# Kernel tuning notes

Hardware: AMD Instinct MI355X
Metric: run time of the kernel (lower is better)

Reference implementation:

```python
import jax, jax.numpy as jnp
import numpy as np

DIM = 1024
NUM_EXPERTS = 8
ACTIVE_EXPERTS = 2
EXPERT_DIM = 2048


def setup_inputs() -> dict:
    key = jax.random.key(0)
    k1, k2, k3, k4 = jax.random.split(key, 4)
    x = jax.random.normal(k1, (1, 2048, DIM), dtype=jnp.float32)
    gate_w = jax.random.normal(k2, (NUM_EXPERTS, DIM), dtype=jnp.float32) * 0.02
    balance_bias = jnp.zeros((NUM_EXPERTS,), dtype=jnp.float32)
    w1 = jax.random.normal(k3, (NUM_EXPERTS, EXPERT_DIM, DIM), dtype=jnp.float32) * 0.02
    w2 = jax.random.normal(k4, (NUM_EXPERTS, DIM, EXPERT_DIM), dtype=jnp.float32) * 0.02
    return {"x": x, "gate_w": gate_w, "balance_bias": balance_bias, "w1": w1, "w2": w2}


def reference(x, gate_w, balance_bias, w1, w2):
    B, S, D = x.shape
    T = B * S
    xf = x.reshape(T, D)
    # gating: sigmoid scores with load-balance bias, then top-k
    gate_logits = jnp.einsum('td,ed->te', xf, gate_w)
    gate_scores = jax.nn.sigmoid(gate_logits + balance_bias)
    topk_scores, topk_idx = jax.lax.top_k(gate_scores, ACTIVE_EXPERTS)
    topk_scores = topk_scores / (topk_scores.sum(axis=-1, keepdims=True) + 1e-6)
    # scatter normalized scores into dense combine weights [T, E]
    comb = jnp.zeros((T, NUM_EXPERTS), dtype=x.dtype)
    comb = comb.at[jnp.arange(T)[:, None], topk_idx].add(topk_scores)
    # expert FFNs (dense over experts; combine weight zeroes unselected)
    h = jax.nn.silu(jnp.einsum('td,ehd->teh', xf, w1))   # [T, E, expert_dim]
    expert_out = jnp.einsum('teh,edh->ted', h, w2)        # [T, E, D]
    out = jnp.einsum('te,ted->td', comb, expert_out)
    return out.reshape(B, S, D)
```

## Files before the change

### kernel.cpp

```cpp
#include <hip/hip_runtime.h>

#define T 2048
#define DIM 1024
#define NE 8
#define ED 2048
#define PSLOT 5120
#define MT_MAX 16

#define BM 128
#define BN 64
#define BK 32

typedef __attribute__((ext_vector_type(8))) short s8v;
typedef __attribute__((ext_vector_type(4))) float f32x4;

__device__ __forceinline__ short f2bf(float f) {
    union { float f; unsigned u; } v;
    v.f = f;
    unsigned r = 0x7FFFu + ((v.u >> 16) & 1u);
    v.u += r;
    return (short)(v.u >> 16);
}

__device__ __forceinline__ float bf2f(short s) {
    union { unsigned u; float f; } v;
    v.u = ((unsigned)(unsigned short)s) << 16;
    return v.f;
}

__device__ __forceinline__ unsigned pkbf2(float lo, float hi) {
    union { float f; unsigned u; } a, b;
    a.f = lo; b.f = hi;
    return __builtin_amdgcn_perm(b.u + 0x8000u, a.u + 0x8000u, 0x07060302u);
}

__device__ __forceinline__ void glds16(const void* g, void* l) {
    __builtin_amdgcn_global_load_lds(
        (const __attribute__((address_space(1))) void*)g,
        (__attribute__((address_space(3))) void*)l, 16, 0, 0);
}

__global__ __launch_bounds__(256) void convert1_kernel(const float* __restrict__ w1,
                                                       short* __restrict__ wbt) {
    int wid = blockIdx.x * 4 + (threadIdx.x >> 6);
    int lane = threadIdx.x & 63;
    int e = wid >> 10, rem = wid & 1023, nb = rem >> 5, kk = rem & 31;
    const float4* src = (const float4*)(w1 + ((size_t)(e * ED + nb * 64 + lane)) * DIM + kk * 32);
    short* dst = wbt + ((size_t)(e * 32 + nb) * 128 + kk * 4) * 512 + lane * 8;
#pragma unroll
    for (int q = 0; q < 4; ++q) {
        float4 f0 = src[2 * q], f1 = src[2 * q + 1];
        uint4 o = { pkbf2(f0.x, f0.y), pkbf2(f0.z, f0.w), pkbf2(f1.x, f1.y), pkbf2(f1.z, f1.w) };
        *(uint4*)(dst + q * 512) = o;
    }
}

__global__ __launch_bounds__(256) void convert2_kernel(const float* __restrict__ w2,
                                                       short* __restrict__ wbt) {
    int wid = blockIdx.x * 4 + (threadIdx.x >> 6);
    int lane = threadIdx.x & 63;
    int e = wid >> 10, rem = wid & 1023, nb = rem >> 6, kk = rem & 63;
    const float4* src = (const float4*)(w2 + ((size_t)(e * DIM + nb * 64 + lane)) * ED + kk * 32);
    short* dst = wbt + ((size_t)(e * 16 + nb) * 256 + kk * 4) * 512 + lane * 8;
#pragma unroll
    for (int q = 0; q < 4; ++q) {
        float4 f0 = src[2 * q], f1 = src[2 * q + 1];
        uint4 o = { pkbf2(f0.x, f0.y), pkbf2(f0.z, f0.w), pkbf2(f1.x, f1.y), pkbf2(f1.z, f1.w) };
        *(uint4*)(dst + q * 512) = o;
    }
}

__global__ void router_kernel(const float* __restrict__ x,
                              const float* __restrict__ gw,
                              const float* __restrict__ bias,
                              int* __restrict__ counts,
                              int* __restrict__ top2i,
                              float* __restrict__ top2w) {
    int wid = threadIdx.x >> 6;
    int lane = threadIdx.x & 63;
    int t = blockIdx.x * 4 + wid;

    const float* xr = x + (size_t)t * DIM + lane * 16;
    float4 xv[4];
#pragma unroll
    for (int j = 0; j < 4; ++j) xv[j] = *(const float4*)(xr + j * 4);

    float sc[NE];
#pragma unroll
    for (int e = 0; e < NE; ++e) {
        const float* gr = gw + e * DIM + lane * 16;
        float p = 0.f;
#pragma unroll
        for (int j = 0; j < 4; ++j) {
            float4 g = *(const float4*)(gr + j * 4);
            p += xv[j].x * g.x + xv[j].y * g.y + xv[j].z * g.z + xv[j].w * g.w;
        }
#pragma unroll
        for (int off = 32; off; off >>= 1) p += __shfl_xor(p, off, 64);
        sc[e] = 1.f / (1.f + __expf(-(p + bias[e])));
    }
    int b0 = 0; float s0 = sc[0];
#pragma unroll
    for (int e = 1; e < NE; ++e) if (sc[e] > s0) { s0 = sc[e]; b0 = e; }
    int b1 = -1; float s1 = -1e30f;
#pragma unroll
    for (int e = 0; e < NE; ++e) if (e != b0 && sc[e] > s1) { s1 = sc[e]; b1 = e; }
    float inv = 1.f / (s0 + s1 + 1e-6f);
    if (lane == 0) {
        top2i[t * 2 + 0] = b0; top2i[t * 2 + 1] = b1;
        top2w[t * 2 + 0] = s0 * inv; top2w[t * 2 + 1] = s1 * inv;
        atomicAdd(&counts[b0], 1);
        atomicAdd(&counts[b1], 1);
    }
}

__global__ __launch_bounds__(256) void plan_kernel(
    const int* __restrict__ counts, const int* __restrict__ top2i,
    int* __restrict__ poff, int* __restrict__ tok_list, int* __restrict__ slot_of) {
    __shared__ int soff[NE];
    __shared__ int srun[NE];
    if (threadIdx.x == 0) {
        int a = 0;
        for (int e = 0; e < NE; ++e) {
            soff[e] = a; poff[e] = a;
            a += ((counts[e] + 127) >> 7) << 7;
            srun[e] = 0;
        }
    }
    __syncthreads();
    for (int t = threadIdx.x; t < T; t += 256) {
#pragma unroll
        for (int k = 0; k < 2; ++k) {
            int e = top2i[t * 2 + k];
            int pos = atomicAdd(&srun[e], 1);
            int slot = soff[e] + pos;
            tok_list[slot] = t;
            slot_of[t * 2 + k] = slot;
        }
    }
    __syncthreads();
    for (int e = 0; e < NE; ++e) {
        int cnt = counts[e];
        int lim = ((cnt + 127) >> 7) << 7;
        for (int i = cnt + threadIdx.x; i < lim; i += 256) tok_list[soff[e] + i] = 0;
    }
}

__global__ __launch_bounds__(256) void gather_kernel(
    const float* __restrict__ x, const int* __restrict__ counts,
    const int* __restrict__ poff, const int* __restrict__ tok_list,
    short* __restrict__ xgt) {
    int e = blockIdx.x, mb = blockIdx.y;
    int cnt = counts[e];
    int mt = (cnt + 127) >> 7;
    if (mb >= mt) return;
    int pb = (poff[e] >> 7) + mb;
    int r = threadIdx.x & 127, hh = threadIdx.x >> 7;
    int tok = tok_list[poff[e] + mb * 128 + r];
    const float4* src = (const float4*)(x + (size_t)tok * DIM + hh * 16);
    short* dst = xgt + ((size_t)pb * 128 + hh * 2) * 1024 + r * 8;
#pragma unroll 4
    for (int kk = 0; kk < DIM / 32; ++kk) {
        float4 f0 = src[0], f1 = src[1], f2 = src[2], f3 = src[3];
        uint4 o0 = { pkbf2(f0.x, f0.y), pkbf2(f0.z, f0.w), pkbf2(f1.x, f1.y), pkbf2(f1.z, f1.w) };
        uint4 o1 = { pkbf2(f2.x, f2.y), pkbf2(f2.z, f2.w), pkbf2(f3.x, f3.y), pkbf2(f3.z, f3.w) };
        *(uint4*)(dst) = o0;
        *(uint4*)(dst + 1024) = o1;
        src += 8;
        dst += 4 * 1024;
    }
}

__global__ __launch_bounds__(256) void ffn1_kernel(
    const short* __restrict__ xgt, const short* __restrict__ wbt,
    const int* __restrict__ counts, const int* __restrict__ poff,
    short* __restrict__ ht) {
    int e = blockIdx.x & 7;
    int j = blockIdx.x >> 3;
    int cnt = counts[e];
    int mt = (cnt + 127) >> 7;
    const int NT = ED / BN;
    if (j >= mt * NT) return;
    int mb = j / NT, nb = j % NT;
    int pb = (poff[e] >> 7) + mb;

    __shared__ __align__(16) short As[2][4][BM][8];
    __shared__ __align__(16) short Bs[2][4][BN][8];

    int tid = threadIdx.x;
    int lane = tid & 63, w = tid >> 6;
    int mo = w * 32;
    int lrow = lane & 15, lq = lane >> 4;

    f32x4 acc[2][4];
#pragma unroll
    for (int mi = 0; mi < 2; ++mi)
#pragma unroll
        for (int ni = 0; ni < 4; ++ni) acc[mi][ni] = (f32x4){0.f, 0.f, 0.f, 0.f};

    const short* asrc = xgt + (size_t)pb * 128 * 1024;
    const short* bsrc = wbt + (size_t)(e * 32 + nb) * 128 * 512;

    auto stage = [&](int s, int b) {
        int p = s * 4 + w;
        glds16(asrc + (size_t)p * 1024 + lane * 8,       &As[b][w][0][0]);
        glds16(asrc + (size_t)p * 1024 + 512 + lane * 8, &As[b][w][64][0]);
        glds16(bsrc + (size_t)p * 512 + lane * 8,        &Bs[b][w][0][0]);
    };
    const int NK = DIM / BK;
    stage(0, 0);
    for (int kk = 0; kk < NK; ++kk) {
        int cur = kk & 1, nxt = cur ^ 1;
        __syncthreads();
        if (kk + 1 < NK) stage(kk + 1, nxt);
        s8v af[2], bfr[4];
#pragma unroll
        for (int mi = 0; mi < 2; ++mi) af[mi] = *(const s8v*)&As[cur][lq][mo + mi * 16 + lrow][0];
#pragma unroll
        for (int ni = 0; ni < 4; ++ni) bfr[ni] = *(const s8v*)&Bs[cur][lq][ni * 16 + lrow][0];
#pragma unroll
        for (int mi = 0; mi < 2; ++mi)
#pragma unroll
            for (int ni = 0; ni < 4; ++ni)
                acc[mi][ni] = __builtin_amdgcn_mfma_f32_16x16x32_bf16(af[mi], bfr[ni], acc[mi][ni], 0, 0, 0);
    }

    int m0 = mb * 128;
#pragma unroll
    for (int mi = 0; mi < 2; ++mi) {
#pragma unroll
        for (int ni = 0; ni < 4; ++ni) {
            int ln = nb * 64 + ni * 16 + lrow;
            int koct = ln >> 3, jj = ln & 7;
#pragma unroll
            for (int r = 0; r < 4; ++r) {
                int lr = mo + mi * 16 + lq * 4 + r;
                if (m0 + lr < cnt) {
                    float v = acc[mi][ni][r];
                    v = v / (1.f + __expf(-v));
                    ht[((size_t)pb * 256 + koct) * 1024 + lr * 8 + jj] = f2bf(v);
                }
            }
        }
    }
}

__global__ __launch_bounds__(256) void ffn2_kernel(
    const short* __restrict__ ht, const short* __restrict__ wbt,
    const int* __restrict__ counts, const int* __restrict__ poff,
    short* __restrict__ eo) {
    int e = blockIdx.x & 7;
    int j = blockIdx.x >> 3;
    int cnt = counts[e];
    int mt = (cnt + 127) >> 7;
    const int NT = DIM / BN;
    if (j >= mt * NT) return;
    int mb = j / NT, nb = j % NT;
    int pb = (poff[e] >> 7) + mb;

    __shared__ __align__(16) short As[2][4][BM][8];
    __shared__ __align__(16) short Bs[2][4][BN][8];

    int tid = threadIdx.x;
    int lane = tid & 63, w = tid >> 6;
    int mo = w * 32;
    int lrow = lane & 15, lq = lane >> 4;

    f32x4 acc[2][4];
#pragma unroll
    for (int mi = 0; mi < 2; ++mi)
#pragma unroll
        for (int ni = 0; ni < 4; ++ni) acc[mi][ni] = (f32x4){0.f, 0.f, 0.f, 0.f};

    const short* asrc = ht + (size_t)pb * 256 * 1024;
    const short* bsrc = wbt + (size_t)(e * 16 + nb) * 256 * 512;

    auto stage = [&](int s, int b) {
        int p = s * 4 + w;
        glds16(asrc + (size_t)p * 1024 + lane * 8,       &As[b][w][0][0]);
        glds16(asrc + (size_t)p * 1024 + 512 + lane * 8, &As[b][w][64][0]);
        glds16(bsrc + (size_t)p * 512 + lane * 8,        &Bs[b][w][0][0]);
    };
    const int NK = ED / BK;
    stage(0, 0);
    for (int kk = 0; kk < NK; ++kk) {
        int cur = kk & 1, nxt = cur ^ 1;
        __syncthreads();
        if (kk + 1 < NK) stage(kk + 1, nxt);
        s8v af[2], bfr[4];
#pragma unroll
        for (int mi = 0; mi < 2; ++mi) af[mi] = *(const s8v*)&As[cur][lq][mo + mi * 16 + lrow][0];
#pragma unroll
        for (int ni = 0; ni < 4; ++ni) bfr[ni] = *(const s8v*)&Bs[cur][lq][ni * 16 + lrow][0];
#pragma unroll
        for (int mi = 0; mi < 2; ++mi)
#pragma unroll
            for (int ni = 0; ni < 4; ++ni)
                acc[mi][ni] = __builtin_amdgcn_mfma_f32_16x16x32_bf16(af[mi], bfr[ni], acc[mi][ni], 0, 0, 0);
    }

    int m0 = mb * 128;
#pragma unroll
    for (int mi = 0; mi < 2; ++mi) {
#pragma unroll
        for (int ni = 0; ni < 4; ++ni) {
            int ln = nb * 64 + ni * 16 + lrow;
#pragma unroll
            for (int r = 0; r < 4; ++r) {
                int lr = mo + mi * 16 + lq * 4 + r;
                if (m0 + lr < cnt) {
                    eo[((size_t)pb * 128 + lr) * 1024 + ln] = f2bf(acc[mi][ni][r]);
                }
            }
        }
    }
}

__global__ __launch_bounds__(256) void combine_kernel(
    const short* __restrict__ eo, const int* __restrict__ slot_of,
    const float* __restrict__ top2w, float* __restrict__ out) {
    int idx = blockIdx.x * 256 + threadIdx.x;
    int t = idx >> 7;
    int c = idx & 127;
    int s0 = slot_of[2 * t], s1 = slot_of[2 * t + 1];
    float w0 = top2w[2 * t], w1 = top2w[2 * t + 1];
    s8v a0 = *(const s8v*)(eo + (size_t)s0 * DIM + c * 8);
    s8v b0 = *(const s8v*)(eo + (size_t)s1 * DIM + c * 8);
    float4 o[2];
#pragma unroll
    for (int j = 0; j < 8; ++j) {
        float v = w0 * bf2f(a0[j]) + w1 * bf2f(b0[j]);
        ((float*)o)[j] = v;
    }
    float4* op = (float4*)(out + (size_t)t * DIM + c * 8);
    op[0] = o[0];
    op[1] = o[1];
}

extern "C" void kernel_launch(void* const* d_in, const int* in_sizes, int n_in,
                              void* d_out, int out_size, void* d_ws, size_t ws_size,
                              hipStream_t stream) {
    const float* x    = (const float*)d_in[0];
    const float* gw   = (const float*)d_in[1];
    const float* bias = (const float*)d_in[2];
    const float* w1   = (const float*)d_in[3];
    const float* w2   = (const float*)d_in[4];
    float* out = (float*)d_out;

    char* ws = (char*)d_ws;
    short* xgt = (short*)ws;
    short* eo  = xgt;
    short* ht  = (short*)(ws + 10485760ull);
    char* meta = ws + 31457280ull;
    int*   counts   = (int*)(meta);
    int*   poff     = (int*)(meta + 64);
    int*   tok_list = (int*)(meta + 128);
    int*   slot_of  = (int*)(meta + 128 + 4 * PSLOT);
    int*   top2i    = (int*)(meta + 128 + 4 * PSLOT + 8 * T);
    float* top2w    = (float*)(meta + 128 + 4 * PSLOT + 16 * T);
    short* wbt = (short*)(ws + 33554432ull);

    hipMemsetAsync(counts, 0, 32, stream);

    convert1_kernel<<<2048, 256, 0, stream>>>(w1, wbt);
    router_kernel<<<T / 4, 256, 0, stream>>>(x, gw, bias, counts, top2i, top2w);
    plan_kernel<<<1, 256, 0, stream>>>(counts, top2i, poff, tok_list, slot_of);
    gather_kernel<<<dim3(NE, MT_MAX), 256, 0, stream>>>(x, counts, poff, tok_list, xgt);
    ffn1_kernel<<<NE * MT_MAX * (ED / BN), 256, 0, stream>>>(xgt, wbt, counts, poff, ht);
    convert2_kernel<<<2048, 256, 0, stream>>>(w2, wbt);
    ffn2_kernel<<<NE * MT_MAX * (DIM / BN), 256, 0, stream>>>(ht, wbt, counts, poff, eo);
    combine_kernel<<<T * DIM / 8 / 256, 256, 0, stream>>>(eo, slot_of, top2w, out);
}
```

Before: 345.1 us.

## Widen GEMM tiles to 128x128, split-K ffn2 and fuse combine via atomics

Widens the N tile of both expert GEMMs from 64 to 128, with a 2x2 warp layout where each warp holds a 64x64 accumulator, and reorders the bf16 weight layout to match. This raises operand reuse per LDS load. ffn2 now splits K in two and scatters weighted results straight into the zeroed fp32 output with atomicAdd, which removes the eo buffer and the separate combine kernel. The cost is a memset of the output, many float atomics, more accumulator registers (lower occupancy), and summation order that is no longer deterministic.

```diff
diff --git a/kernel.cpp b/kernel.cpp
--- a/kernel.cpp
+++ b/kernel.cpp
@@ -8,7 +8,7 @@
 #define MT_MAX 16
 
 #define BM 128
-#define BN 64
+#define BN 128
 #define BK 32
 
 typedef __attribute__((ext_vector_type(8))) short s8v;
@@ -44,14 +44,15 @@
                                                        short* __restrict__ wbt) {
     int wid = blockIdx.x * 4 + (threadIdx.x >> 6);
     int lane = threadIdx.x & 63;
-    int e = wid >> 10, rem = wid & 1023, nb = rem >> 5, kk = rem & 31;
-    const float4* src = (const float4*)(w1 + ((size_t)(e * ED + nb * 64 + lane)) * DIM + kk * 32);
-    short* dst = wbt + ((size_t)(e * 32 + nb) * 128 + kk * 4) * 512 + lane * 8;
+    int e = wid >> 10, rem = wid & 1023;
+    int nb = rem >> 6, h = (rem >> 5) & 1, kk = rem & 31;
+    const float4* src = (const float4*)(w1 + ((size_t)(e * ED + nb * 128 + h * 64 + lane)) * DIM + kk * 32);
+    short* dst = wbt + ((size_t)(e * 16 + nb) * 128 + kk * 4) * 1024 + h * 512 + lane * 8;
 #pragma unroll
     for (int q = 0; q < 4; ++q) {
         float4 f0 = src[2 * q], f1 = src[2 * q + 1];
         uint4 o = { pkbf2(f0.x, f0.y), pkbf2(f0.z, f0.w), pkbf2(f1.x, f1.y), pkbf2(f1.z, f1.w) };
-        *(uint4*)(dst + q * 512) = o;
+        *(uint4*)(dst + q * 1024) = o;
     }
 }
 
@@ -59,14 +60,15 @@
                                                        short* __restrict__ wbt) {
     int wid = blockIdx.x * 4 + (threadIdx.x >> 6);
     int lane = threadIdx.x & 63;
-    int e = wid >> 10, rem = wid & 1023, nb = rem >> 6, kk = rem & 63;
-    const float4* src = (const float4*)(w2 + ((size_t)(e * DIM + nb * 64 + lane)) * ED + kk * 32);
-    short* dst = wbt + ((size_t)(e * 16 + nb) * 256 + kk * 4) * 512 + lane * 8;
+    int e = wid >> 10, rem = wid & 1023;
+    int nb = rem >> 7, h = (rem >> 6) & 1, kk = rem & 63;
+    const float4* src = (const float4*)(w2 + ((size_t)(e * DIM + nb * 128 + h * 64 + lane)) * ED + kk * 32);
+    short* dst = wbt + ((size_t)(e * 8 + nb) * 256 + kk * 4) * 1024 + h * 512 + lane * 8;
 #pragma unroll
     for (int q = 0; q < 4; ++q) {
         float4 f0 = src[2 * q], f1 = src[2 * q + 1];
         uint4 o = { pkbf2(f0.x, f0.y), pkbf2(f0.z, f0.w), pkbf2(f1.x, f1.y), pkbf2(f1.z, f1.w) };
-        *(uint4*)(dst + q * 512) = o;
+        *(uint4*)(dst + q * 1024) = o;
     }
 }
 
@@ -116,7 +118,8 @@
 
 __global__ __launch_bounds__(256) void plan_kernel(
     const int* __restrict__ counts, const int* __restrict__ top2i,
-    int* __restrict__ poff, int* __restrict__ tok_list, int* __restrict__ slot_of) {
+    const float* __restrict__ top2w,
+    int* __restrict__ poff, int* __restrict__ tok_list, float* __restrict__ slot_w) {
     __shared__ int soff[NE];
     __shared__ int srun[NE];
     if (threadIdx.x == 0) {
@@ -135,14 +138,17 @@
             int pos = atomicAdd(&srun[e], 1);
             int slot = soff[e] + pos;
             tok_list[slot] = t;
-            slot_of[t * 2 + k] = slot;
+            slot_w[slot] = top2w[t * 2 + k];
         }
     }
     __syncthreads();
     for (int e = 0; e < NE; ++e) {
         int cnt = counts[e];
         int lim = ((cnt + 127) >> 7) << 7;
-        for (int i = cnt + threadIdx.x; i < lim; i += 256) tok_list[soff[e] + i] = 0;
+        for (int i = cnt + threadIdx.x; i < lim; i += 256) {
+            tok_list[soff[e] + i] = 0;
+            slot_w[soff[e] + i] = 0.f;
+        }
     }
 }
 
@@ -189,23 +195,24 @@
 
     int tid = threadIdx.x;
     int lane = tid & 63, w = tid >> 6;
-    int mo = w * 32;
+    int mo = (w >> 1) * 64, no = (w & 1) * 64;
     int lrow = lane & 15, lq = lane >> 4;
 
-    f32x4 acc[2][4];
-#pragma unroll
-    for (int mi = 0; mi < 2; ++mi)
+    f32x4 acc[4][4];
+#pragma unroll
+    for (int mi = 0; mi < 4; ++mi)
 #pragma unroll
         for (int ni = 0; ni < 4; ++ni) acc[mi][ni] = (f32x4){0.f, 0.f, 0.f, 0.f};
 
     const short* asrc = xgt + (size_t)pb * 128 * 1024;
-    const short* bsrc = wbt + (size_t)(e * 32 + nb) * 128 * 512;
+    const short* bsrc = wbt + (size_t)(e * 16 + nb) * 128 * 1024;
 
     auto stage = [&](int s, int b) {
         int p = s * 4 + w;
         glds16(asrc + (size_t)p * 1024 + lane * 8,       &As[b][w][0][0]);
         glds16(asrc + (size_t)p * 1024 + 512 + lane * 8, &As[b][w][64][0]);
-        glds16(bsrc + (size_t)p * 512 + lane * 8,        &Bs[b][w][0][0]);
+        glds16(bsrc + (size_t)p * 1024 + lane * 8,       &Bs[b][w][0][0]);
+        glds16(bsrc + (size_t)p * 1024 + 512 + lane * 8, &Bs[b][w][64][0]);
     };
     const int NK = DIM / BK;
     stage(0, 0);
@@ -213,13 +220,13 @@
         int cur = kk & 1, nxt = cur ^ 1;
         __syncthreads();
         if (kk + 1 < NK) stage(kk + 1, nxt);
-        s8v af[2], bfr[4];
-#pragma unroll
-        for (int mi = 0; mi < 2; ++mi) af[mi] = *(const s8v*)&As[cur][lq][mo + mi * 16 + lrow][0];
-#pragma unroll
-        for (int ni = 0; ni < 4; ++ni) bfr[ni] = *(const s8v*)&Bs[cur][lq][ni * 16 + lrow][0];
-#pragma unroll
-        for (int mi = 0; mi < 2; ++mi)
+        s8v af[4], bfr[4];
+#pragma unroll
+        for (int mi = 0; mi < 4; ++mi) af[mi] = *(const s8v*)&As[cur][lq][mo + mi * 16 + lrow][0];
+#pragma unroll
+        for (int ni = 0; ni < 4; ++ni) bfr[ni] = *(const s8v*)&Bs[cur][lq][no + ni * 16 + lrow][0];
+#pragma unroll
+        for (int mi = 0; mi < 4; ++mi)
 #pragma unroll
             for (int ni = 0; ni < 4; ++ni)
                 acc[mi][ni] = __builtin_amdgcn_mfma_f32_16x16x32_bf16(af[mi], bfr[ni], acc[mi][ni], 0, 0, 0);
@@ -227,10 +234,10 @@
 
     int m0 = mb * 128;
 #pragma unroll
-    for (int mi = 0; mi < 2; ++mi) {
+    for (int mi = 0; mi < 4; ++mi) {
 #pragma unroll
         for (int ni = 0; ni < 4; ++ni) {
-            int ln = nb * 64 + ni * 16 + lrow;
+            int ln = nb * 128 + no + ni * 16 + lrow;
             int koct = ln >> 3, jj = ln & 7;
 #pragma unroll
             for (int r = 0; r < 4; ++r) {
@@ -248,13 +255,15 @@
 __global__ __launch_bounds__(256) void ffn2_kernel(
     const short* __restrict__ ht, const short* __restrict__ wbt,
     const int* __restrict__ counts, const int* __restrict__ poff,
-    short* __restrict__ eo) {
+    const int* __restrict__ tok_list, const float* __restrict__ slot_w,
+    float* __restrict__ out) {
     int e = blockIdx.x & 7;
     int j = blockIdx.x >> 3;
     int cnt = counts[e];
     int mt = (cnt + 127) >> 7;
     const int NT = DIM / BN;
-    if (j >= mt * NT) return;
+    if (j >= mt * NT * 2) return;
+    int ksp = j & 1; j >>= 1;
     int mb = j / NT, nb = j % NT;
     int pb = (poff[e] >> 7) + mb;
 
@@ -263,37 +272,38 @@
 
     int tid = threadIdx.x;
     int lane = tid & 63, w = tid >> 6;
-    int mo = w * 32;
+    int mo = (w >> 1) * 64, no = (w & 1) * 64;
     int lrow = lane & 15, lq = lane >> 4;
 
-    f32x4 acc[2][4];
-#pragma unroll
-    for (int mi = 0; mi < 2; ++mi)
+    f32x4 acc[4][4];
+#pragma unroll
+    for (int mi = 0; mi < 4; ++mi)
 #pragma unroll
         for (int ni = 0; ni < 4; ++ni) acc[mi][ni] = (f32x4){0.f, 0.f, 0.f, 0.f};
 
-    const short* asrc = ht + (size_t)pb * 256 * 1024;
-    const short* bsrc = wbt + (size_t)(e * 16 + nb) * 256 * 512;
+    const short* asrc = ht + ((size_t)pb * 256 + ksp * 128) * 1024;
+    const short* bsrc = wbt + ((size_t)(e * 8 + nb) * 256 + ksp * 128) * 1024;
 
     auto stage = [&](int s, int b) {
         int p = s * 4 + w;
         glds16(asrc + (size_t)p * 1024 + lane * 8,       &As[b][w][0][0]);
         glds16(asrc + (size_t)p * 1024 + 512 + lane * 8, &As[b][w][64][0]);
-        glds16(bsrc + (size_t)p * 512 + lane * 8,        &Bs[b][w][0][0]);
+        glds16(bsrc + (size_t)p * 1024 + lane * 8,       &Bs[b][w][0][0]);
+        glds16(bsrc + (size_t)p * 1024 + 512 + lane * 8, &Bs[b][w][64][0]);
     };
-    const int NK = ED / BK;
+    const int NK = (ED / 2) / BK;
     stage(0, 0);
     for (int kk = 0; kk < NK; ++kk) {
         int cur = kk & 1, nxt = cur ^ 1;
         __syncthreads();
         if (kk + 1 < NK) stage(kk + 1, nxt);
-        s8v af[2], bfr[4];
-#pragma unroll
-        for (int mi = 0; mi < 2; ++mi) af[mi] = *(const s8v*)&As[cur][lq][mo + mi * 16 + lrow][0];
-#pragma unroll
-        for (int ni = 0; ni < 4; ++ni) bfr[ni] = *(const s8v*)&Bs[cur][lq][ni * 16 + lrow][0];
-#pragma unroll
-        for (int mi = 0; mi < 2; ++mi)
+        s8v af[4], bfr[4];
+#pragma unroll
+        for (int mi = 0; mi < 4; ++mi) af[mi] = *(const s8v*)&As[cur][lq][mo + mi * 16 + lrow][0];
+#pragma unroll
+        for (int ni = 0; ni < 4; ++ni) bfr[ni] = *(const s8v*)&Bs[cur][lq][no + ni * 16 + lrow][0];
+#pragma unroll
+        for (int mi = 0; mi < 4; ++mi)
 #pragma unroll
             for (int ni = 0; ni < 4; ++ni)
                 acc[mi][ni] = __builtin_amdgcn_mfma_f32_16x16x32_bf16(af[mi], bfr[ni], acc[mi][ni], 0, 0, 0);
@@ -301,40 +311,21 @@
 
     int m0 = mb * 128;
 #pragma unroll
-    for (int mi = 0; mi < 2; ++mi) {
-#pragma unroll
-        for (int ni = 0; ni < 4; ++ni) {
-            int ln = nb * 64 + ni * 16 + lrow;
-#pragma unroll
-            for (int r = 0; r < 4; ++r) {
-                int lr = mo + mi * 16 + lq * 4 + r;
-                if (m0 + lr < cnt) {
-                    eo[((size_t)pb * 128 + lr) * 1024 + ln] = f2bf(acc[mi][ni][r]);
-                }
+    for (int mi = 0; mi < 4; ++mi) {
+#pragma unroll
+        for (int r = 0; r < 4; ++r) {
+            int lr = mo + mi * 16 + lq * 4 + r;
+            if (m0 + lr < cnt) {
+                int slot = poff[e] + m0 + lr;
+                int t = tok_list[slot];
+                float wv = slot_w[slot];
+                float* orow = out + (size_t)t * DIM + nb * 128 + no + lrow;
+#pragma unroll
+                for (int ni = 0; ni < 4; ++ni)
+                    atomicAdd(orow + ni * 16, wv * acc[mi][ni][r]);
             }
         }
     }
-}
-
-__global__ __launch_bounds__(256) void combine_kernel(
-    const short* __restrict__ eo, const int* __restrict__ slot_of,
-    const float* __restrict__ top2w, float* __restrict__ out) {
-    int idx = blockIdx.x * 256 + threadIdx.x;
-    int t = idx >> 7;
-    int c = idx & 127;
-    int s0 = slot_of[2 * t], s1 = slot_of[2 * t + 1];
-    float w0 = top2w[2 * t], w1 = top2w[2 * t + 1];
-    s8v a0 = *(const s8v*)(eo + (size_t)s0 * DIM + c * 8);
-    s8v b0 = *(const s8v*)(eo + (size_t)s1 * DIM + c * 8);
-    float4 o[2];
-#pragma unroll
-    for (int j = 0; j < 8; ++j) {
-        float v = w0 * bf2f(a0[j]) + w1 * bf2f(b0[j]);
-        ((float*)o)[j] = v;
-    }
-    float4* op = (float4*)(out + (size_t)t * DIM + c * 8);
-    op[0] = o[0];
-    op[1] = o[1];
 }
 
 extern "C" void kernel_launch(void* const* d_in, const int* in_sizes, int n_in,
@@ -348,26 +339,25 @@
     float* out = (float*)d_out;
 
     char* ws = (char*)d_ws;
-    short* xgt = (short*)ws;
-    short* eo  = xgt;
-    short* ht  = (short*)(ws + 10485760ull);
+    short* ht  = (short*)ws;
+    short* xgt = (short*)(ws + 20971520ull);
     char* meta = ws + 31457280ull;
     int*   counts   = (int*)(meta);
     int*   poff     = (int*)(meta + 64);
     int*   tok_list = (int*)(meta + 128);
-    int*   slot_of  = (int*)(meta + 128 + 4 * PSLOT);
-    int*   top2i    = (int*)(meta + 128 + 4 * PSLOT + 8 * T);
-    float* top2w    = (float*)(meta + 128 + 4 * PSLOT + 16 * T);
+    float* slot_w   = (float*)(meta + 128 + 4 * PSLOT);
+    int*   top2i    = (int*)(meta + 128 + 8 * PSLOT);
+    float* top2w    = (float*)(meta + 128 + 8 * PSLOT + 8 * T);
     short* wbt = (short*)(ws + 33554432ull);
 
     hipMemsetAsync(counts, 0, 32, stream);
+    hipMemsetAsync(out, 0, (size_t)T * DIM * 4, stream);
 
     convert1_kernel<<<2048, 256, 0, stream>>>(w1, wbt);
     router_kernel<<<T / 4, 256, 0, stream>>>(x, gw, bias, counts, top2i, top2w);
-    plan_kernel<<<1, 256, 0, stream>>>(counts, top2i, poff, tok_list, slot_of);
+    plan_kernel<<<1, 256, 0, stream>>>(counts, top2i, top2w, poff, tok_list, slot_w);
     gather_kernel<<<dim3(NE, MT_MAX), 256, 0, stream>>>(x, counts, poff, tok_list, xgt);
     ffn1_kernel<<<NE * MT_MAX * (ED / BN), 256, 0, stream>>>(xgt, wbt, counts, poff, ht);
     convert2_kernel<<<2048, 256, 0, stream>>>(w2, wbt);
-    ffn2_kernel<<<NE * MT_MAX * (DIM / BN), 256, 0, stream>>>(ht, wbt, counts, poff, eo);
-    combine_kernel<<<T * DIM / 8 / 256, 256, 0, stream>>>(eo, slot_of, top2w, out);
-}
+    ffn2_kernel<<<NE * MT_MAX * (DIM / BN) * 2, 256, 0, stream>>>(ht, wbt, counts, poff, tok_list, slot_w, out);
+}
```

After: 343.4 us. No clear change (-0.5%).
